# Optimization experiments

Hardware: AMD Instinct MI355X
Metric: run time of the kernel (lower is better)

## Reference

```python
import jax, jax.numpy as jnp
import numpy as np

N_QUBITS = 8
N_LAYERS = 2
DIM = 2 ** N_QUBITS  # 256


def _ry(theta):
    h = theta * 0.5
    c, s = jnp.cos(h), jnp.sin(h)
    return jnp.stack([jnp.stack([c, -s]), jnp.stack([s, c])]).astype(jnp.complex64)


def _rz(theta):
    e = jnp.exp(-0.5j * theta.astype(jnp.complex64))
    z = jnp.zeros((), jnp.complex64)
    return jnp.stack([jnp.stack([e, z]), jnp.stack([z, jnp.conj(e)])])


def _apply_1q(state, U, w):
    # state: (2,)*n tensor, wire 0 = most significant (PennyLane convention)
    s = jnp.moveaxis(state, w, 0)
    s = jnp.tensordot(U, s, axes=((1,), (0,)))
    return jnp.moveaxis(s, 0, w)


def _cnot(state, c, t):
    s = jnp.moveaxis(state, (c, t), (0, 1))
    s = jnp.stack([s[0, 0], s[0, 1], s[1, 1], s[1, 0]]).reshape((2, 2) + s.shape[2:])
    return jnp.moveaxis(s, (0, 1), (c, t))


def _conv_pair(state, q1, q2, p):
    state = _apply_1q(state, _ry(p[0]), q1)
    state = _apply_1q(state, _ry(p[1]), q2)
    state = _cnot(state, q1, q2)
    state = _apply_1q(state, _ry(p[2]), q1)
    state = _apply_1q(state, _ry(p[3]), q2)
    state = _cnot(state, q2, q1)
    return state


def _circuit(angles, node_idx, adj, qp):
    n = N_QUBITS
    state = jnp.zeros((2,) * n, jnp.complex64).at[(0,) * n].set(1.0)
    a = jnp.clip(angles, -np.pi, np.pi)
    # angle encoding: RY on all wires, RZ on wires 0..n/2-1
    for i in range(n):
        state = _apply_1q(state, _ry(a[i]), i)
    for i in range(n // 2):
        state = _apply_1q(state, _rz(a[i + n // 2]), i)
    # graph-structure entanglement: conditional CNOT(c=node%n, t) if adj[c,t]>0
    c = (node_idx % n).astype(jnp.int32)
    adj_row = adj[c]
    flat = state.reshape(-1)
    idx = jnp.arange(DIM, dtype=jnp.int32)
    bit_c = (idx >> (n - 1 - c)) & 1  # dynamic control wire
    for t in range(n):
        perm = idx ^ (bit_c << (n - 1 - t))
        cond = (adj_row[t] > 0) & (t != c)
        flat = jnp.where(cond, flat[perm], flat)
    state = flat.reshape((2,) * n)
    # quantum conv layers
    ppc = 4 * (n - 1)
    off = 0
    for _ in range(N_LAYERS):
        p = qp[off:off + ppc]
        k = 0
        for i in range(0, n - 1, 2):
            state = _conv_pair(state, i, i + 1, p[k:k + 4]); k += 4
        for i in range(1, n - 1, 2):
            state = _conv_pair(state, i, i + 1, p[k:k + 4]); k += 4
        off += ppc
    # pooling rotations on even wires
    pool = qp[off:off + n]
    for q in range(0, n, 2):
        state = _apply_1q(state, _ry(pool[q]), q)
    # <Z_w> expectation values
    probs = jnp.abs(state) ** 2
    z = jnp.stack([probs.take(0, axis=w).sum() - probs.take(1, axis=w).sum()
                   for w in range(n)])
    return z


def setup_inputs() -> dict:
    key = jax.random.key(0)
    ks = jax.random.split(key, 12)
    B, S, N, F = 64, 12, 207, 2
    x = jax.random.normal(ks[0], (B, S, N, F), jnp.float32)
    adj = jax.random.randint(ks[1], (N, N), 0, 2).astype(jnp.float32)
    w_proj = jax.random.normal(ks[2], (N_QUBITS, S * F), jnp.float32) * 0.1
    b_proj = jax.random.normal(ks[3], (N_QUBITS,), jnp.float32) * 0.1
    q_params = jax.random.normal(ks[4], (4 * (N_QUBITS - 1) * N_LAYERS + N_QUBITS,), jnp.float32) * 0.1
    w1 = jax.random.normal(ks[5], (64, N_QUBITS), jnp.float32) * 0.1
    b1 = jax.random.normal(ks[6], (64,), jnp.float32) * 0.1
    w2 = jax.random.normal(ks[7], (32, 64), jnp.float32) * 0.1
    b2 = jax.random.normal(ks[8], (32,), jnp.float32) * 0.1
    w3 = jax.random.normal(ks[9], (1, 32), jnp.float32) * 0.1
    b3 = jax.random.normal(ks[10], (1,), jnp.float32) * 0.1
    return dict(x=x, adj=adj, w_proj=w_proj, b_proj=b_proj, q_params=q_params,
                w1=w1, b1=b1, w2=w2, b2=b2, w3=w3, b3=b3)


def reference(x, adj, w_proj, b_proj, q_params, w1, b1, w2, b2, w3, b3):
    B, S, N, F = x.shape
    feats = jnp.transpose(x, (0, 2, 1, 3)).reshape(B, N, S * F)
    angles = feats @ w_proj.T + b_proj                      # (B, N, 8)
    node_idx = jnp.tile(jnp.arange(N, dtype=jnp.int32), B)  # (B*N,)
    z = jax.vmap(_circuit, in_axes=(0, 0, None, None))(
        angles.reshape(B * N, N_QUBITS), node_idx, adj, q_params)
    # original detaches quantum features before the classical head
    z = jax.lax.stop_gradient(z).reshape(B, N, N_QUBITS).astype(jnp.float32)
    h = jax.nn.relu(z @ w1.T + b1)   # dropout is identity in eval mode
    h = jax.nn.relu(h @ w2.T + b2)
    out = h @ w3.T + b3              # (B, N, 1)
    return out.squeeze(-1)
```

## Files before the change

### kernel.cpp

```cpp
#include <hip/hip_runtime.h>
#include <math.h>

#define DEV static __device__ __forceinline__

constexpr int SS = 12;
constexpr int NN = 207;
constexpr int NCIRC = 64 * NN;
constexpr int NPAIR = NCIRC / 2;


typedef float v2f __attribute__((ext_vector_type(2)));
typedef float v4f __attribute__((ext_vector_type(4)));

DEV v2f splat2(float x) { v2f r; r.x = x; r.y = x; return r; }
DEV v2f vfma(float m, v2f a, v2f acc) { return __builtin_elementwise_fma(splat2(m), a, acc); }
DEV v2f vmul(float m, v2f a) { return splat2(m) * a; }
template<int M> DEV float sxc(float v) { return __shfl_xor(v, M, 64); }
template<int M> DEV v2f sx2(v2f v) { v2f r; r.x = sxc<M>(v.x); r.y = sxc<M>(v.y); return r; }
DEV float bperm(int addr, float v) {
    return __int_as_float(__builtin_amdgcn_ds_bpermute(addr, __float_as_int(v)));
}

#define CONV4(P, x00, x01, x10, x11) do {                                  \
    v2f _b00 = x00, _b01 = x01, _b10 = x10, _b11 = x11;                    \
    x00 = vfma((P)[0],  _b00, vfma((P)[1],  _b01, vfma((P)[2],  _b10, vmul((P)[3],  _b11)))); \
    x01 = vfma((P)[4],  _b00, vfma((P)[5],  _b01, vfma((P)[6],  _b10, vmul((P)[7],  _b11)))); \
    x10 = vfma((P)[8],  _b00, vfma((P)[9],  _b01, vfma((P)[10], _b10, vmul((P)[11], _b11)))); \
    x11 = vfma((P)[12], _b00, vfma((P)[13], _b01, vfma((P)[14], _b10, vmul((P)[15], _b11)))); \
} while (0)

#define CONVM10(P) do { CONV4(P, a0, a1, a2, a3); CONV4(P, a4, a5, a6, a7); } while (0)
#define CONVM02(P) do { CONV4(P, a0, a4, a1, a5); CONV4(P, a2, a6, a3, a7); } while (0)
#define CONVM21(P) do { CONV4(P, a0, a2, a4, a6); CONV4(P, a1, a3, a5, a7); } while (0)

#define SWP(ML, lb, lo, hi) do {                                           \
    v2f _u = (lb) ? lo : hi;                                               \
    v2f _v = sx2<ML>(_u);                                                  \
    lo = (lb) ? _v : lo;                                                   \
    hi = (lb) ? hi : _v;                                                   \
} while (0)

#define SWKL0(LB) do { const bool _lb = (lane >> (LB)) & 1;                \
    SWP(1 << (LB), _lb, a0, a1); SWP(1 << (LB), _lb, a2, a3);              \
    SWP(1 << (LB), _lb, a4, a5); SWP(1 << (LB), _lb, a6, a7); } while (0)
#define SWKL1(LB) do { const bool _lb = (lane >> (LB)) & 1;                \
    SWP(1 << (LB), _lb, a0, a2); SWP(1 << (LB), _lb, a1, a3);              \
    SWP(1 << (LB), _lb, a4, a6); SWP(1 << (LB), _lb, a5, a7); } while (0)
#define SWKL2(LB) do { const bool _lb = (lane >> (LB)) & 1;                \
    SWP(1 << (LB), _lb, a0, a4); SWP(1 << (LB), _lb, a1, a5);              \
    SWP(1 << (LB), _lb, a2, a6); SWP(1 << (LB), _lb, a3, a7); } while (0)

template<int MK> DEV float whts(float p, int lane) {
    float t = sxc<MK>(p);
    return (lane & MK) ? (t - p) : (p + t);
}

__global__ void prep_kernel(const float* __restrict__ qp, float* __restrict__ ws) {
    const int n = threadIdx.x;
    if (n >= 14) return;
    const int Jt[14] = {12, 8, 24, 4, 20, 0, 16, 28, 32, 44, 36, 48, 40, 52};
    const int J = Jt[n];
    float cg[4], sg[4];
    for (int i = 0; i < 4; i++) sincosf(0.5f * qp[J + i], &sg[i], &cg[i]);
    float A[16], B[16], M[16];
    {
        float H[2][2] = {{cg[0], -sg[0]}, {sg[0], cg[0]}};
        float L[2][2] = {{cg[1], -sg[1]}, {sg[1], cg[1]}};
        for (int a_ = 0; a_ < 2; a_++) for (int b_ = 0; b_ < 2; b_++)
            for (int p = 0; p < 2; p++) for (int q = 0; q < 2; q++)
                A[(2*a_+b_)*4 + (2*p+q)] = H[a_][p] * L[b_][q];
    }
    for (int j = 0; j < 4; j++) { float t = A[8+j]; A[8+j] = A[12+j]; A[12+j] = t; }
    {
        float H[2][2] = {{cg[2], -sg[2]}, {sg[2], cg[2]}};
        float L[2][2] = {{cg[3], -sg[3]}, {sg[3], cg[3]}};
        for (int a_ = 0; a_ < 2; a_++) for (int b_ = 0; b_ < 2; b_++)
            for (int p = 0; p < 2; p++) for (int q = 0; q < 2; q++)
                B[(2*a_+b_)*4 + (2*p+q)] = H[a_][p] * L[b_][q];
    }
    for (int r = 0; r < 4; r++)
        for (int c = 0; c < 4; c++) {
            float acc = 0.0f;
            for (int k = 0; k < 4; k++) acc += B[r*4+k] * A[k*4+c];
            M[r*4+c] = acc;
        }
    for (int j = 0; j < 4; j++) { float t = M[4+j]; M[4+j] = M[12+j]; M[12+j] = t; }
    int mode = 0; float fc = 1.0f, fs = 0.0f;
    if (n == 7)  { sincosf(0.5f * qp[56], &fs, &fc); mode = 2; }
    if (n == 9)  { sincosf(0.5f * qp[58], &fs, &fc); mode = 1; }
    if (n == 11) { sincosf(0.5f * qp[60], &fs, &fc); mode = 1; }
    if (n == 13) { sincosf(0.5f * qp[62], &fs, &fc); mode = 1; }
    if (mode == 1) {
        for (int j = 0; j < 4; j++) {
            float r0 = M[j],     r1 = M[4+j];
            M[j]    = fc * r0 - fs * r1;  M[4+j]  = fs * r0 + fc * r1;
            float r2 = M[8+j],   r3 = M[12+j];
            M[8+j]  = fc * r2 - fs * r3;  M[12+j] = fs * r2 + fc * r3;
        }
    } else if (mode == 2) {
        for (int j = 0; j < 4; j++) {
            float r0 = M[j],     r2 = M[8+j];
            M[j]    = fc * r0 - fs * r2;  M[8+j]  = fs * r0 + fc * r2;
            float r1 = M[4+j],   r3 = M[12+j];
            M[4+j]  = fc * r1 - fs * r3;  M[12+j] = fs * r1 + fc * r3;
        }
    }
    for (int i = 0; i < 16; i++) ws[16*n + i] = M[i];
}

__global__ __launch_bounds__(256, 6) void qcnn_kernel(
    const float* __restrict__ x, const float* __restrict__ adj,
    const float* __restrict__ w_proj, const float* __restrict__ b_proj,
    const float* __restrict__ ws,
    const float* __restrict__ w1, const float* __restrict__ b1,
    const float* __restrict__ w2, const float* __restrict__ b2,
    const float* __restrict__ w3, const float* __restrict__ b3,
    float* __restrict__ out)
{
    const int lane = threadIdx.x & 63;
    const int half = lane >> 5;
    const int hl   = lane & 31;
    const int wv   = threadIdx.x >> 6;
    const int gA   = blockIdx.x * 4 + wv;
    const int bA   = gA / NN;
    const int node = gA - bA * NN;
    const int bb   = bA + (half << 5);

    const float* xp = x + ((size_t)bb * SS * NN + node) * 2;
    v2f av0 = splat2(0.0f), av1 = av0, av2 = av0, av3 = av0,
        av4 = av0, av5 = av0, av6 = av0, av7 = av0;
#pragma unroll
    for (int s = 0; s < SS; s++) {
        const v2f xv = *(const v2f*)(xp + (size_t)s * (NN * 2));
        const float* wp = w_proj + 2 * s;
        av0 = __builtin_elementwise_fma(xv, *(const v2f*)(wp + 0 * 24), av0);
        av1 = __builtin_elementwise_fma(xv, *(const v2f*)(wp + 1 * 24), av1);
        av2 = __builtin_elementwise_fma(xv, *(const v2f*)(wp + 2 * 24), av2);
        av3 = __builtin_elementwise_fma(xv, *(const v2f*)(wp + 3 * 24), av3);
        av4 = __builtin_elementwise_fma(xv, *(const v2f*)(wp + 4 * 24), av4);
        av5 = __builtin_elementwise_fma(xv, *(const v2f*)(wp + 5 * 24), av5);
        av6 = __builtin_elementwise_fma(xv, *(const v2f*)(wp + 6 * 24), av6);
        av7 = __builtin_elementwise_fma(xv, *(const v2f*)(wp + 7 * 24), av7);
    }
    const float PI_F = 3.14159265358979323846f;
    float ang0 = fminf(fmaxf(av0.x + av0.y + b_proj[0], -PI_F), PI_F);
    float ang1 = fminf(fmaxf(av1.x + av1.y + b_proj[1], -PI_F), PI_F);
    float ang2 = fminf(fmaxf(av2.x + av2.y + b_proj[2], -PI_F), PI_F);
    float ang3 = fminf(fmaxf(av3.x + av3.y + b_proj[3], -PI_F), PI_F);
    float ang4 = fminf(fmaxf(av4.x + av4.y + b_proj[4], -PI_F), PI_F);
    float ang5 = fminf(fmaxf(av5.x + av5.y + b_proj[5], -PI_F), PI_F);
    float ang6 = fminf(fmaxf(av6.x + av6.y + b_proj[6], -PI_F), PI_F);
    float ang7 = fminf(fmaxf(av7.x + av7.y + b_proj[7], -PI_F), PI_F);

    float c0, s0, c1, s1, c2, s2, c3, s3, c4, s4, c5, s5, c6, s6, c7, s7;
    __sincosf(0.5f * ang0, &s0, &c0); __sincosf(0.5f * ang1, &s1, &c1);
    __sincosf(0.5f * ang2, &s2, &c2); __sincosf(0.5f * ang3, &s3, &c3);
    __sincosf(0.5f * ang4, &s4, &c4); __sincosf(0.5f * ang5, &s5, &c5);
    __sincosf(0.5f * ang6, &s6, &c6); __sincosf(0.5f * ang7, &s7, &c7);
    float A = (((lane >> 4) & 1) ? s0 : c0) * (((lane >> 3) & 1) ? s1 : c1)
            * (((lane >> 2) & 1) ? s2 : c2) * (((lane >> 1) & 1) ? s3 : c3)
            * (((lane >> 0) & 1) ? s4 : c4);
    float phi = (((lane >> 4) & 1) ? 0.5f : -0.5f) * ang4
              + (((lane >> 3) & 1) ? 0.5f : -0.5f) * ang5
              + (((lane >> 2) & 1) ? 0.5f : -0.5f) * ang6
              + (((lane >> 1) & 1) ? 0.5f : -0.5f) * ang7;
    float cp, sp;
    __sincosf(phi, &sp, &cp);
    v2f ph; ph.x = cp; ph.y = sp;

    const float c5c6 = c5 * c6, c5s6 = c5 * s6, s5c6 = s5 * c6, s5s6 = s5 * s6;
    v2f a0 = vmul(A * c5c6 * c7, ph), a1 = vmul(A * c5c6 * s7, ph);
    v2f a2 = vmul(A * c5s6 * c7, ph), a3 = vmul(A * c5s6 * s7, ph);
    v2f a4 = vmul(A * s5c6 * c7, ph), a5 = vmul(A * s5c6 * s7, ph);
    v2f a6 = vmul(A * s5s6 * c7, ph), a7 = vmul(A * s5s6 * s7, ph);

    const int cq = node & 7;
    int M = 0;
#pragma unroll
    for (int t = 0; t < 8; t++) {
        float avv = adj[cq * NN + t];
        if (t != cq && avv > 0.0f) M |= 1 << (7 - t);
    }
    if (M) {
        const int Mlo = M & 7;
        const int Mhi = (M >> 3) & 31;
        v2f p0, p1, p2, p3, p4, p5, p6, p7;
        switch (Mlo) {
        case 0: p0=a0;p1=a1;p2=a2;p3=a3;p4=a4;p5=a5;p6=a6;p7=a7; break;
        case 1: p0=a1;p1=a0;p2=a3;p3=a2;p4=a5;p5=a4;p6=a7;p7=a6; break;
        case 2: p0=a2;p1=a3;p2=a0;p3=a1;p4=a6;p5=a7;p6=a4;p7=a5; break;
        case 3: p0=a3;p1=a2;p2=a1;p3=a0;p4=a7;p5=a6;p6=a5;p7=a4; break;
        case 4: p0=a4;p1=a5;p2=a6;p3=a7;p4=a0;p5=a1;p6=a2;p7=a3; break;
        case 5: p0=a5;p1=a4;p2=a7;p3=a6;p4=a1;p5=a0;p6=a3;p7=a2; break;
        case 6: p0=a6;p1=a7;p2=a4;p3=a5;p4=a2;p5=a3;p6=a0;p7=a1; break;
        default:p0=a7;p1=a6;p2=a5;p3=a4;p4=a3;p5=a2;p6=a1;p7=a0; break;
        }
        const int addr = (lane ^ Mhi) << 2;
        p0.x = bperm(addr, p0.x); p0.y = bperm(addr, p0.y);
        p1.x = bperm(addr, p1.x); p1.y = bperm(addr, p1.y);
        p2.x = bperm(addr, p2.x); p2.y = bperm(addr, p2.y);
        p3.x = bperm(addr, p3.x); p3.y = bperm(addr, p3.y);
        p4.x = bperm(addr, p4.x); p4.y = bperm(addr, p4.y);
        p5.x = bperm(addr, p5.x); p5.y = bperm(addr, p5.y);
        p6.x = bperm(addr, p6.x); p6.y = bperm(addr, p6.y);
        p7.x = bperm(addr, p7.x); p7.y = bperm(addr, p7.y);
        const int pc = 7 - cq;
        if (pc >= 3) {
            const bool bs = (lane >> (pc - 3)) & 1;
            a0 = bs ? p0 : a0; a1 = bs ? p1 : a1; a2 = bs ? p2 : a2; a3 = bs ? p3 : a3;
            a4 = bs ? p4 : a4; a5 = bs ? p5 : a5; a6 = bs ? p6 : a6; a7 = bs ? p7 : a7;
        } else if (pc == 2) { a4 = p4; a5 = p5; a6 = p6; a7 = p7; }
        else if (pc == 1)   { a2 = p2; a3 = p3; a6 = p6; a7 = p7; }
        else                { a1 = p1; a3 = p3; a5 = p5; a7 = p7; }
    }

    CONVM10(ws + 0);
    SWKL0(0);
    CONVM02(ws + 16);
    CONVM21(ws + 32);
    SWKL2(2);
    SWKL1(1);
    CONVM21(ws + 48);
    CONVM10(ws + 64);
    SWKL0(3);
    SWKL1(4);
    CONVM10(ws + 80);
    CONVM02(ws + 96);
    CONVM10(ws + 112);
    SWKL1(4);
    CONVM21(ws + 128);
    CONVM02(ws + 144);
    SWKL0(3);
    SWKL2(2);
    CONVM02(ws + 160);
    CONVM10(ws + 176);
    SWKL1(1);
    SWKL0(0);
    CONVM10(ws + 192);
    CONVM21(ws + 208);

    const float q0 = fmaf(a0.x, a0.x, a0.y * a0.y);
    const float q1 = fmaf(a1.x, a1.x, a1.y * a1.y);
    const float q2 = fmaf(a2.x, a2.x, a2.y * a2.y);
    const float q3 = fmaf(a3.x, a3.x, a3.y * a3.y);
    const float q4 = fmaf(a4.x, a4.x, a4.y * a4.y);
    const float q5 = fmaf(a5.x, a5.x, a5.y * a5.y);
    const float q6 = fmaf(a6.x, a6.x, a6.y * a6.y);
    const float q7 = fmaf(a7.x, a7.x, a7.y * a7.y);
    const float t0 = q0 + q1, t1 = q2 + q3, t2 = q4 + q5, t3 = q6 + q7;
    v2f z76;
    z76.x = ((q0 - q1) + (q2 - q3)) + ((q4 - q5) + (q6 - q7));
    z76.y = (t0 - t1) + (t2 - t3);
    float z5p = (t0 + t1) - (t2 + t3);
    float w   = (t0 + t1) + (t2 + t3);
    z76 += sx2<1>(z76);  z76 += sx2<2>(z76);  z76 += sx2<4>(z76);
    z76 += sx2<8>(z76);  z76 += sx2<16>(z76);
    z5p += sxc<1>(z5p);  z5p += sxc<2>(z5p);  z5p += sxc<4>(z5p);
    z5p += sxc<8>(z5p);  z5p += sxc<16>(z5p);
    w = whts<1>(w, lane); w = whts<2>(w, lane); w = whts<4>(w, lane);
    w = whts<8>(w, lane); w = whts<16>(w, lane);
    const int gb = (lane & 32) << 2;
    const float z4 = bperm(gb | (1 << 2),  w);
    const float z3 = bperm(gb | (2 << 2),  w);
    const float z2 = bperm(gb | (4 << 2),  w);
    const float z1 = bperm(gb | (8 << 2),  w);
    const float z0 = bperm(gb | (16 << 2), w);
    v4f zlo; zlo.x = z0; zlo.y = z1; zlo.z = z2;    zlo.w = z3;
    v4f zhi; zhi.x = z4; zhi.y = z5p; zhi.z = z76.y; zhi.w = z76.x;

    const v4f* r0 = (const v4f*)(w1 + hl * 8);
    const v4f* r1 = (const v4f*)(w1 + (hl + 32) * 8);
    v4f ha = zlo * r0[0]; ha = __builtin_elementwise_fma(zhi, r0[1], ha);
    v4f hb = zlo * r1[0]; hb = __builtin_elementwise_fma(zhi, r1[1], hb);
    const float h1a = fmaxf(b1[hl]      + (ha.x + ha.y) + (ha.z + ha.w), 0.0f);
    const float h1b = fmaxf(b1[hl + 32] + (hb.x + hb.y) + (hb.z + hb.w), 0.0f);

    __shared__ float h1s[4][2][64];
    h1s[wv][half][hl]      = h1a;
    h1s[wv][half][hl + 32] = h1b;

    const v4f* hv  = (const v4f*)(&h1s[wv][half][0]);
    const v4f* w2r = (const v4f*)(w2 + hl * 64);
    v4f acc = {0.0f, 0.0f, 0.0f, 0.0f};
#pragma unroll
    for (int j = 0; j < 16; j++)
        acc = __builtin_elementwise_fma(hv[j], w2r[j], acc);
    const float h2 = fmaxf(b2[hl] + (acc.x + acc.y) + (acc.z + acc.w), 0.0f);

    float o = h2 * w3[hl];
    o += sxc<1>(o); o += sxc<2>(o); o += sxc<4>(o); o += sxc<8>(o); o += sxc<16>(o);

    if (hl == 0) out[gA + half * NPAIR] = o + b3[0];
}

extern "C" void kernel_launch(void* const* d_in, const int* in_sizes, int n_in,
                              void* d_out, int out_size, void* d_ws, size_t ws_size,
                              hipStream_t stream) {
    const float* x      = (const float*)d_in[0];
    const float* adj    = (const float*)d_in[1];
    const float* w_proj = (const float*)d_in[2];
    const float* b_proj = (const float*)d_in[3];
    const float* qp     = (const float*)d_in[4];
    const float* w1     = (const float*)d_in[5];
    const float* b1     = (const float*)d_in[6];
    const float* w2     = (const float*)d_in[7];
    const float* b2     = (const float*)d_in[8];
    const float* w3     = (const float*)d_in[9];
    const float* b3     = (const float*)d_in[10];
    float* out = (float*)d_out;
    float* ws  = (float*)d_ws;

    hipLaunchKernelGGL(prep_kernel, dim3(1), dim3(64), 0, stream, qp, ws);
    hipLaunchKernelGGL(qcnn_kernel, dim3(NPAIR / 4), dim3(256), 0, stream,
                       x, adj, w_proj, b_proj, ws, w1, b1, w2, b2, w3, b3, out);
}
```

Baseline: 100.9 us.

## Hoist per-circuit angle projection and sincos into prep kernel

Moves the per-circuit input projection, clamping and eight sincos evaluations out of the main kernel. Previously all 32 lanes of a half-wave redundantly computed them; now they run once per circuit in an expanded prep kernel (53 blocks) and are written to the workspace. The CNOT adjacency masks are also precomputed per control wire, and the main kernel's launch bound rises from 6 to 7 blocks per SM. The trade-off is an extra global round-trip of 24 floats per circuit and a larger prep launch on the critical path.

```diff
diff --git a/kernel.cpp b/kernel.cpp
--- a/kernel.cpp
+++ b/kernel.cpp
@@ -55,8 +55,63 @@
     return (lane & MK) ? (t - p) : (p + t);
 }
 
-__global__ void prep_kernel(const float* __restrict__ qp, float* __restrict__ ws) {
+__global__ void prep_kernel(const float* __restrict__ x, const float* __restrict__ adj,
+                            const float* __restrict__ w_proj, const float* __restrict__ b_proj,
+                            const float* __restrict__ qp, float* __restrict__ ws) {
+    if (blockIdx.x < 52) {
+        const int t = blockIdx.x * 256 + threadIdx.x;
+        if (t >= NCIRC) return;
+        const int b = t / NN, node = t - b * NN;
+        const float* xp = x + ((size_t)b * SS * NN + node) * 2;
+        v2f av0 = splat2(0.0f), av1 = av0, av2 = av0, av3 = av0,
+            av4 = av0, av5 = av0, av6 = av0, av7 = av0;
+#pragma unroll
+        for (int s = 0; s < SS; s++) {
+            const v2f xv = *(const v2f*)(xp + (size_t)s * (NN * 2));
+            const float* wp = w_proj + 2 * s;
+            av0 = __builtin_elementwise_fma(xv, *(const v2f*)(wp + 0 * 24), av0);
+            av1 = __builtin_elementwise_fma(xv, *(const v2f*)(wp + 1 * 24), av1);
+            av2 = __builtin_elementwise_fma(xv, *(const v2f*)(wp + 2 * 24), av2);
+            av3 = __builtin_elementwise_fma(xv, *(const v2f*)(wp + 3 * 24), av3);
+            av4 = __builtin_elementwise_fma(xv, *(const v2f*)(wp + 4 * 24), av4);
+            av5 = __builtin_elementwise_fma(xv, *(const v2f*)(wp + 5 * 24), av5);
+            av6 = __builtin_elementwise_fma(xv, *(const v2f*)(wp + 6 * 24), av6);
+            av7 = __builtin_elementwise_fma(xv, *(const v2f*)(wp + 7 * 24), av7);
+        }
+        const float PI_F = 3.14159265358979323846f;
+        const float ang0 = fminf(fmaxf(av0.x + av0.y + b_proj[0], -PI_F), PI_F);
+        const float ang1 = fminf(fmaxf(av1.x + av1.y + b_proj[1], -PI_F), PI_F);
+        const float ang2 = fminf(fmaxf(av2.x + av2.y + b_proj[2], -PI_F), PI_F);
+        const float ang3 = fminf(fmaxf(av3.x + av3.y + b_proj[3], -PI_F), PI_F);
+        const float ang4 = fminf(fmaxf(av4.x + av4.y + b_proj[4], -PI_F), PI_F);
+        const float ang5 = fminf(fmaxf(av5.x + av5.y + b_proj[5], -PI_F), PI_F);
+        const float ang6 = fminf(fmaxf(av6.x + av6.y + b_proj[6], -PI_F), PI_F);
+        const float ang7 = fminf(fmaxf(av7.x + av7.y + b_proj[7], -PI_F), PI_F);
+        float c0,s0,c1,s1,c2,s2,c3,s3,c4,s4,c5,s5,c6,s6,c7,s7;
+        __sincosf(0.5f * ang0, &s0, &c0); __sincosf(0.5f * ang1, &s1, &c1);
+        __sincosf(0.5f * ang2, &s2, &c2); __sincosf(0.5f * ang3, &s3, &c3);
+        __sincosf(0.5f * ang4, &s4, &c4); __sincosf(0.5f * ang5, &s5, &c5);
+        __sincosf(0.5f * ang6, &s6, &c6); __sincosf(0.5f * ang7, &s7, &c7);
+        float* dst = ws + 256 + (size_t)t * 24;
+        dst[0] = c0;  dst[1] = c1;  dst[2] = c2;  dst[3] = c3;
+        dst[4] = c4;  dst[5] = c5;  dst[6] = c6;  dst[7] = c7;
+        dst[8] = s0;  dst[9] = s1;  dst[10] = s2; dst[11] = s3;
+        dst[12] = s4; dst[13] = s5; dst[14] = s6; dst[15] = s7;
+        dst[16] = ang4; dst[17] = ang5; dst[18] = ang6; dst[19] = ang7;
+        return;
+    }
     const int n = threadIdx.x;
+    if (n >= 14 && n < 64 + 14) {
+        const int cq = n - 14;
+        if (cq < 8) {
+            int M = 0;
+            for (int t = 0; t < 8; t++) {
+                if (t != cq && adj[cq * NN + t] > 0.0f) M |= 1 << (7 - t);
+            }
+            ((int*)ws)[224 + cq] = M;
+        }
+        return;
+    }
     if (n >= 14) return;
     const int Jt[14] = {12, 8, 24, 4, 20, 0, 16, 28, 32, 44, 36, 48, 40, 52};
     const int J = Jt[n];
@@ -108,9 +163,7 @@
     for (int i = 0; i < 16; i++) ws[16*n + i] = M[i];
 }
 
-__global__ __launch_bounds__(256, 6) void qcnn_kernel(
-    const float* __restrict__ x, const float* __restrict__ adj,
-    const float* __restrict__ w_proj, const float* __restrict__ b_proj,
+__global__ __launch_bounds__(256, 7) void qcnn_kernel(
     const float* __restrict__ ws,
     const float* __restrict__ w1, const float* __restrict__ b1,
     const float* __restrict__ w2, const float* __restrict__ b2,
@@ -124,63 +177,35 @@
     const int gA   = blockIdx.x * 4 + wv;
     const int bA   = gA / NN;
     const int node = gA - bA * NN;
-    const int bb   = bA + (half << 5);
-
-    const float* xp = x + ((size_t)bb * SS * NN + node) * 2;
-    v2f av0 = splat2(0.0f), av1 = av0, av2 = av0, av3 = av0,
-        av4 = av0, av5 = av0, av6 = av0, av7 = av0;
-#pragma unroll
-    for (int s = 0; s < SS; s++) {
-        const v2f xv = *(const v2f*)(xp + (size_t)s * (NN * 2));
-        const float* wp = w_proj + 2 * s;
-        av0 = __builtin_elementwise_fma(xv, *(const v2f*)(wp + 0 * 24), av0);
-        av1 = __builtin_elementwise_fma(xv, *(const v2f*)(wp + 1 * 24), av1);
-        av2 = __builtin_elementwise_fma(xv, *(const v2f*)(wp + 2 * 24), av2);
-        av3 = __builtin_elementwise_fma(xv, *(const v2f*)(wp + 3 * 24), av3);
-        av4 = __builtin_elementwise_fma(xv, *(const v2f*)(wp + 4 * 24), av4);
-        av5 = __builtin_elementwise_fma(xv, *(const v2f*)(wp + 5 * 24), av5);
-        av6 = __builtin_elementwise_fma(xv, *(const v2f*)(wp + 6 * 24), av6);
-        av7 = __builtin_elementwise_fma(xv, *(const v2f*)(wp + 7 * 24), av7);
-    }
-    const float PI_F = 3.14159265358979323846f;
-    float ang0 = fminf(fmaxf(av0.x + av0.y + b_proj[0], -PI_F), PI_F);
-    float ang1 = fminf(fmaxf(av1.x + av1.y + b_proj[1], -PI_F), PI_F);
-    float ang2 = fminf(fmaxf(av2.x + av2.y + b_proj[2], -PI_F), PI_F);
-    float ang3 = fminf(fmaxf(av3.x + av3.y + b_proj[3], -PI_F), PI_F);
-    float ang4 = fminf(fmaxf(av4.x + av4.y + b_proj[4], -PI_F), PI_F);
-    float ang5 = fminf(fmaxf(av5.x + av5.y + b_proj[5], -PI_F), PI_F);
-    float ang6 = fminf(fmaxf(av6.x + av6.y + b_proj[6], -PI_F), PI_F);
-    float ang7 = fminf(fmaxf(av7.x + av7.y + b_proj[7], -PI_F), PI_F);
-
-    float c0, s0, c1, s1, c2, s2, c3, s3, c4, s4, c5, s5, c6, s6, c7, s7;
-    __sincosf(0.5f * ang0, &s0, &c0); __sincosf(0.5f * ang1, &s1, &c1);
-    __sincosf(0.5f * ang2, &s2, &c2); __sincosf(0.5f * ang3, &s3, &c3);
-    __sincosf(0.5f * ang4, &s4, &c4); __sincosf(0.5f * ang5, &s5, &c5);
-    __sincosf(0.5f * ang6, &s6, &c6); __sincosf(0.5f * ang7, &s7, &c7);
-    float A = (((lane >> 4) & 1) ? s0 : c0) * (((lane >> 3) & 1) ? s1 : c1)
-            * (((lane >> 2) & 1) ? s2 : c2) * (((lane >> 1) & 1) ? s3 : c3)
-            * (((lane >> 0) & 1) ? s4 : c4);
-    float phi = (((lane >> 4) & 1) ? 0.5f : -0.5f) * ang4
-              + (((lane >> 3) & 1) ? 0.5f : -0.5f) * ang5
-              + (((lane >> 2) & 1) ? 0.5f : -0.5f) * ang6
-              + (((lane >> 1) & 1) ? 0.5f : -0.5f) * ang7;
+    const int g    = gA + half * NPAIR;
+
+    const float* cd = ws + 256 + (size_t)g * 24;
+    const v4f cA = *(const v4f*)(cd + 0);
+    const v4f cB = *(const v4f*)(cd + 4);
+    const v4f sA = *(const v4f*)(cd + 8);
+    const v4f sB = *(const v4f*)(cd + 12);
+    const v4f rz = *(const v4f*)(cd + 16);
+
+    const float A = (((lane >> 4) & 1) ? sA.x : cA.x) * (((lane >> 3) & 1) ? sA.y : cA.y)
+                  * (((lane >> 2) & 1) ? sA.z : cA.z) * (((lane >> 1) & 1) ? sA.w : cA.w)
+                  * (((lane >> 0) & 1) ? sB.x : cB.x);
+    const float phi = (((lane >> 4) & 1) ? 0.5f : -0.5f) * rz.x
+                    + (((lane >> 3) & 1) ? 0.5f : -0.5f) * rz.y
+                    + (((lane >> 2) & 1) ? 0.5f : -0.5f) * rz.z
+                    + (((lane >> 1) & 1) ? 0.5f : -0.5f) * rz.w;
     float cp, sp;
     __sincosf(phi, &sp, &cp);
     v2f ph; ph.x = cp; ph.y = sp;
 
-    const float c5c6 = c5 * c6, c5s6 = c5 * s6, s5c6 = s5 * c6, s5s6 = s5 * s6;
-    v2f a0 = vmul(A * c5c6 * c7, ph), a1 = vmul(A * c5c6 * s7, ph);
-    v2f a2 = vmul(A * c5s6 * c7, ph), a3 = vmul(A * c5s6 * s7, ph);
-    v2f a4 = vmul(A * s5c6 * c7, ph), a5 = vmul(A * s5c6 * s7, ph);
-    v2f a6 = vmul(A * s5s6 * c7, ph), a7 = vmul(A * s5s6 * s7, ph);
+    const float c5c6 = cB.y * cB.z, c5s6 = cB.y * sB.z;
+    const float s5c6 = sB.y * cB.z, s5s6 = sB.y * sB.z;
+    v2f a0 = vmul(A * c5c6 * cB.w, ph), a1 = vmul(A * c5c6 * sB.w, ph);
+    v2f a2 = vmul(A * c5s6 * cB.w, ph), a3 = vmul(A * c5s6 * sB.w, ph);
+    v2f a4 = vmul(A * s5c6 * cB.w, ph), a5 = vmul(A * s5c6 * sB.w, ph);
+    v2f a6 = vmul(A * s5s6 * cB.w, ph), a7 = vmul(A * s5s6 * sB.w, ph);
 
     const int cq = node & 7;
-    int M = 0;
-#pragma unroll
-    for (int t = 0; t < 8; t++) {
-        float avv = adj[cq * NN + t];
-        if (t != cq && avv > 0.0f) M |= 1 << (7 - t);
-    }
+    const int M = ((const int*)ws)[224 + cq];
     if (M) {
         const int Mlo = M & 7;
         const int Mhi = (M >> 3) & 31;
@@ -265,7 +290,7 @@
     const float z2 = bperm(gb | (4 << 2),  w);
     const float z1 = bperm(gb | (8 << 2),  w);
     const float z0 = bperm(gb | (16 << 2), w);
-    v4f zlo; zlo.x = z0; zlo.y = z1; zlo.z = z2;    zlo.w = z3;
+    v4f zlo; zlo.x = z0; zlo.y = z1;  zlo.z = z2;    zlo.w = z3;
     v4f zhi; zhi.x = z4; zhi.y = z5p; zhi.z = z76.y; zhi.w = z76.x;
 
     const v4f* r0 = (const v4f*)(w1 + hl * 8);
@@ -290,7 +315,7 @@
     float o = h2 * w3[hl];
     o += sxc<1>(o); o += sxc<2>(o); o += sxc<4>(o); o += sxc<8>(o); o += sxc<16>(o);
 
-    if (hl == 0) out[gA + half * NPAIR] = o + b3[0];
+    if (hl == 0) out[g] = o + b3[0];
 }
 
 extern "C" void kernel_launch(void* const* d_in, const int* in_sizes, int n_in,
@@ -310,7 +335,8 @@
     float* out = (float*)d_out;
     float* ws  = (float*)d_ws;
 
-    hipLaunchKernelGGL(prep_kernel, dim3(1), dim3(64), 0, stream, qp, ws);
+    hipLaunchKernelGGL(prep_kernel, dim3(53), dim3(256), 0, stream,
+                       x, adj, w_proj, b_proj, qp, ws);
     hipLaunchKernelGGL(qcnn_kernel, dim3(NPAIR / 4), dim3(256), 0, stream,
-                       x, adj, w_proj, b_proj, ws, w1, b1, w2, b2, w3, b3, out);
-}
+                       ws, w1, b1, w2, b2, w3, b3, out);
+}
```

After: 97.89 us. -3.0%, faster.
